# Performance work log

Hardware: AMD Instinct MI355X
Metric: run time of the kernel (lower is better)

The kernel has to match this reference:

```python
import jax, jax.numpy as jnp
import numpy as np

L = 2        # n_layer
D = 1024     # hidden_size
H = 8        # n_head
DK = D // H  # head_dim = 128
DV = D // H
T = 2048     # max_seq_length
B = 4
INTER = 2816 # fla GatedMLP: int(1024*4*2/3)=2730 rounded up to multiple of 256
EPS = 1e-6


def rmsnorm(x, w):
    return x * jax.lax.rsqrt(jnp.mean(x * x, axis=-1, keepdims=True) + EPS) * w


def l2norm(x):
    return x * jax.lax.rsqrt(jnp.sum(x * x, axis=-1, keepdims=True) + EPS)


def delta_attn(x, Wq, Wk, Wv, Wb, Wo, onorm_w):
    # x: [B, T, D]
    b, t, _ = x.shape
    q = jax.nn.silu((x @ Wq).reshape(b, t, H, DK))
    k = jax.nn.silu((x @ Wk).reshape(b, t, H, DK))
    q = l2norm(q)
    k = l2norm(k)
    v = jax.nn.silu((x @ Wv).reshape(b, t, H, DV))
    beta = jax.nn.sigmoid(x @ Wb) * 2.0  # [B,T,H], allow_neg_eigval=True
    # time-major for scan
    qt = q.transpose(1, 0, 2, 3)  # [T,B,H,DK]
    kt = k.transpose(1, 0, 2, 3)
    vt = v.transpose(1, 0, 2, 3)
    bt = beta.transpose(1, 0, 2)  # [T,B,H]

    def step(S, inps):
        qi, ki, vi, bi = inps
        # delta rule: S_t = S_{t-1} + beta_t * k_t (v_t - S_{t-1}^T k_t)^T
        pred = jnp.einsum('bhkv,bhk->bhv', S, ki)
        S = S + bi[..., None, None] * ki[..., :, None] * (vi - pred)[..., None, :]
        o = jnp.einsum('bhkv,bhk->bhv', S, qi)
        return S, o

    S0 = jnp.zeros((b, H, DK, DV), x.dtype)
    _, o = jax.lax.scan(step, S0, (qt, kt, vt, bt))  # o: [T,B,H,DV]
    o = rmsnorm(o, onorm_w)  # per-head RMSNorm (use_gate=False)
    o = o.transpose(1, 0, 2, 3).reshape(b, t, H * DV)
    return o @ Wo


def setup_inputs() -> dict:
    key = jax.random.key(0)
    ks = jax.random.split(key, 13)
    s = 0.02
    f32 = jnp.float32
    return {
        'input_embeds': jax.random.normal(ks[0], (T, B, D), f32),
        'Wq': jax.random.normal(ks[1], (L, D, D), f32) * s,
        'Wk': jax.random.normal(ks[2], (L, D, D), f32) * s,
        'Wv': jax.random.normal(ks[3], (L, D, D), f32) * s,
        'Wb': jax.random.normal(ks[4], (L, D, H), f32) * s,
        'Wo': jax.random.normal(ks[5], (L, D, D), f32) * s,
        'onorm_w': jnp.ones((L, DV), f32) + jax.random.normal(ks[6], (L, DV), f32) * 0.02,
        'norm1_w': jnp.ones((L, D), f32) + jax.random.normal(ks[7], (L, D), f32) * 0.02,
        'norm2_w': jnp.ones((L, D), f32) + jax.random.normal(ks[8], (L, D), f32) * 0.02,
        'Wg': jax.random.normal(ks[9], (L, D, 2 * INTER), f32) * s,
        'Wd': jax.random.normal(ks[10], (L, INTER, D), f32) * s,
        'final_norm_w': jnp.ones((D,), f32) + jax.random.normal(ks[11], (D,), f32) * 0.02,
    }


def reference(input_embeds, Wq, Wk, Wv, Wb, Wo, onorm_w, norm1_w, norm2_w, Wg, Wd, final_norm_w):
    # wrapper transposes (T,B,D) -> (B,T,D)
    x = input_embeds.transpose(1, 0, 2)
    for l in range(L):
        h = rmsnorm(x, norm1_w[l])
        x = x + delta_attn(h, Wq[l], Wk[l], Wv[l], Wb[l], Wo[l], onorm_w[l])
        h = rmsnorm(x, norm2_w[l])
        gy = h @ Wg[l]
        g, y = jnp.split(gy, 2, axis=-1)
        x = x + (jax.nn.silu(g) * y) @ Wd[l]
    x = rmsnorm(x, final_norm_w)
    return x.transpose(1, 0, 2)  # back to (T,B,D)
```

## Files before the change

kernel.cpp:

```cpp
#include <hip/hip_runtime.h>
#include <hip/hip_bf16.h>
#include <cstdint>


typedef _Float16 f16;
typedef __attribute__((ext_vector_type(8))) _Float16 h8;
typedef __attribute__((ext_vector_type(4))) _Float16 h4;
typedef __attribute__((ext_vector_type(4))) float f4;

#define DEV __device__ __forceinline__

static constexpr int Bb_ = 4;
static constexpr int Hh  = 8;
static constexpr int Dd  = 1024;
static constexpr int Tt  = 2048;
static constexpr int NC  = 32;

DEV float siluf(float x) { return x / (1.f + expf(-x)); }
DEV int swz16(int row, int c) { return (c & 8) | ((c & 7) ^ (row & 7)); }

#define AS1(p) ((const __attribute__((address_space(1))) void*)(uintptr_t)(p))
#define AS3(p) ((__attribute__((address_space(3))) void*)(uint32_t)(uintptr_t)(p))

DEV h8 rd_sw(const f16* T, int row, int chunk) {
  return *(const h8*)(T + (((row << 3) | (chunk ^ (row & 7))) * 8));
}

template<int EPI, int SC>
__global__ __launch_bounds__(512, 2) void gemm2(const f16* __restrict__ A, const f16* __restrict__ Bt,
                                                void* __restrict__ C, const float* __restrict__ rs,
                                                int M, int N, int K, int gx) {
  __shared__ __align__(16) f16 ldsA[2][16384];
  __shared__ __align__(16) f16 ldsB[2][8192];
  const int tid = threadIdx.x, lane = tid & 63, w = tid >> 6;
  const int l15 = lane & 15, l4 = lane >> 4;
  const int wr = w >> 2, wc = w & 3;
  const int nwg = gridDim.x;
  int flat = blockIdx.x;
  if ((nwg & 7) == 0) flat = (flat & 7) * (nwg >> 3) + (flat >> 3);
  const int bx = flat % gx, by = flat / gx;

  const f16* Ab = A + (size_t)by * 256 * K;
  const f16* Bb = Bt + (size_t)bx * 128 * K;
  const int NT = K >> 6;
  f4 acc[8][2] = {};

  const int r0 = tid >> 3;
  const size_t soff0 = (size_t)r0 * K + (size_t)(((tid & 7) ^ (r0 & 7)) * 8);
  const size_t soff1 = soff0 + (size_t)64 * K;
  const int dof = tid * 8;
  auto STG = [&](const f16* base, f16* dst) {
    __builtin_amdgcn_global_load_lds(AS1(base + soff0), AS3(dst + dof), 16, 0, 0);
    __builtin_amdgcn_global_load_lds(AS1(base + soff1), AS3(dst + 4096 + dof), 16, 0, 0);
  };

  STG(Bb, ldsB[0]);
  STG(Ab, ldsA[0]);
  STG(Ab + (size_t)128 * K, ldsA[0] + 8192);
  if (NT > 1) {
    STG(Bb + 64, ldsB[1]);
    asm volatile("s_waitcnt vmcnt(2)");
  } else {
    asm volatile("s_waitcnt vmcnt(0)");
  }
  __builtin_amdgcn_s_barrier();

  for (int t = 0; t < NT; ++t) {
    const int cur = t & 1, nxt = cur ^ 1;
    const f16* cA = ldsA[cur];
    const f16* cB = ldsB[cur];
    h8 b[2][2], aX[2][2], aY[2][2];
#pragma unroll
    for (int cf = 0; cf < 2; ++cf)
#pragma unroll
      for (int ks = 0; ks < 2; ++ks)
        b[cf][ks] = rd_sw(cB, wc * 32 + cf * 16 + l15, ks * 4 + l4);
#pragma unroll
    for (int fr = 0; fr < 2; ++fr)
#pragma unroll
      for (int ks = 0; ks < 2; ++ks)
        aX[fr][ks] = rd_sw(cA, wr * 128 + fr * 16 + l15, ks * 4 + l4);
    if (t + 1 < NT) { STG(Ab + (t + 1) * 64, ldsA[nxt]); STG(Ab + (size_t)128 * K + (t + 1) * 64, ldsA[nxt] + 8192); }
    __builtin_amdgcn_s_setprio(1);
#pragma unroll
    for (int fr = 0; fr < 2; ++fr)
#pragma unroll
      for (int cf = 0; cf < 2; ++cf)
#pragma unroll
        for (int ks = 0; ks < 2; ++ks)
          acc[fr][cf] = __builtin_amdgcn_mfma_f32_16x16x32_f16(aX[fr][ks], b[cf][ks], acc[fr][cf], 0, 0, 0);
#pragma unroll
    for (int fr = 0; fr < 2; ++fr)
#pragma unroll
      for (int ks = 0; ks < 2; ++ks)
        aY[fr][ks] = rd_sw(cA, wr * 128 + 32 + fr * 16 + l15, ks * 4 + l4);
#pragma unroll
    for (int fr = 0; fr < 2; ++fr)
#pragma unroll
      for (int cf = 0; cf < 2; ++cf)
#pragma unroll
        for (int ks = 0; ks < 2; ++ks)
          acc[2 + fr][cf] = __builtin_amdgcn_mfma_f32_16x16x32_f16(aY[fr][ks], b[cf][ks], acc[2 + fr][cf], 0, 0, 0);
    __builtin_amdgcn_s_setprio(0);
    __builtin_amdgcn_s_barrier();
#pragma unroll
    for (int fr = 0; fr < 2; ++fr)
#pragma unroll
      for (int ks = 0; ks < 2; ++ks)
        aX[fr][ks] = rd_sw(cA, wr * 128 + 64 + fr * 16 + l15, ks * 4 + l4);
    if (t + 2 < NT) STG(Bb + (t + 2) * 64, ldsB[cur]);
    __builtin_amdgcn_s_setprio(1);
#pragma unroll
    for (int fr = 0; fr < 2; ++fr)
#pragma unroll
      for (int cf = 0; cf < 2; ++cf)
#pragma unroll
        for (int ks = 0; ks < 2; ++ks)
          acc[4 + fr][cf] = __builtin_amdgcn_mfma_f32_16x16x32_f16(aX[fr][ks], b[cf][ks], acc[4 + fr][cf], 0, 0, 0);
#pragma unroll
    for (int fr = 0; fr < 2; ++fr)
#pragma unroll
      for (int ks = 0; ks < 2; ++ks)
        aY[fr][ks] = rd_sw(cA, wr * 128 + 96 + fr * 16 + l15, ks * 4 + l4);
#pragma unroll
    for (int fr = 0; fr < 2; ++fr)
#pragma unroll
      for (int cf = 0; cf < 2; ++cf)
#pragma unroll
        for (int ks = 0; ks < 2; ++ks)
          acc[6 + fr][cf] = __builtin_amdgcn_mfma_f32_16x16x32_f16(aY[fr][ks], b[cf][ks], acc[6 + fr][cf], 0, 0, 0);
    __builtin_amdgcn_s_setprio(0);
    if (t + 2 < NT)      asm volatile("s_waitcnt vmcnt(2)" ::: "memory");
    else if (t + 1 < NT) asm volatile("s_waitcnt vmcnt(0)" ::: "memory");
    __builtin_amdgcn_s_barrier();
  }

#pragma unroll
  for (int fr = 0; fr < 8; ++fr) {
#pragma unroll
    for (int cf = 0; cf < 2; ++cf) {
      const int row0 = by * 256 + wr * 128 + fr * 16 + l4 * 4;
      const int col = bx * 128 + wc * 32 + cf * 16 + l15;
#pragma unroll
      for (int q = 0; q < 4; ++q) {
        const size_t idx = (size_t)(row0 + q) * N + col;
        float v = acc[fr][cf][q];
        if (SC) v *= rs[row0 + q];
        if (EPI == 1) ((f16*)C)[idx] = (f16)((float)((f16*)C)[idx] + v);
        if (EPI == 2) ((f16*)C)[idx] = (f16)v;
      }
    }
  }
}

__global__ __launch_bounds__(512, 2) void gemmQKV(const f16* __restrict__ A, const f16* __restrict__ Bt,
                                                  const float* __restrict__ rs, f16* __restrict__ qb,
                                                  f16* __restrict__ kb, f16* __restrict__ vb,
                                                  int K, int gx) {
  __shared__ __align__(16) f16 ldsA[2][16384];
  __shared__ __align__(16) f16 ldsB[2][8192];
  __shared__ float ps[4][256];
  const int tid = threadIdx.x, lane = tid & 63, w = tid >> 6;
  const int l15 = lane & 15, l4 = lane >> 4;
  const int wr = w >> 2, wc = w & 3;
  const int nwg = gridDim.x;
  int flat = blockIdx.x;
  if ((nwg & 7) == 0) flat = (flat & 7) * (nwg >> 3) + (flat >> 3);
  const int bx = flat % gx, by = flat / gx;

  const f16* Ab = A + (size_t)by * 256 * K;
  const f16* Bb = Bt + (size_t)bx * 128 * K;
  const int NT = K >> 6;
  f4 acc[8][2] = {};

  const int r0 = tid >> 3;
  const size_t soff0 = (size_t)r0 * K + (size_t)(((tid & 7) ^ (r0 & 7)) * 8);
  const size_t soff1 = soff0 + (size_t)64 * K;
  const int dof = tid * 8;
  auto STG = [&](const f16* base, f16* dst) {
    __builtin_amdgcn_global_load_lds(AS1(base + soff0), AS3(dst + dof), 16, 0, 0);
    __builtin_amdgcn_global_load_lds(AS1(base + soff1), AS3(dst + 4096 + dof), 16, 0, 0);
  };

  STG(Bb, ldsB[0]);
  STG(Ab, ldsA[0]);
  STG(Ab + (size_t)128 * K, ldsA[0] + 8192);
  if (NT > 1) {
    STG(Bb + 64, ldsB[1]);
    asm volatile("s_waitcnt vmcnt(2)");
  } else {
    asm volatile("s_waitcnt vmcnt(0)");
  }
  __builtin_amdgcn_s_barrier();

  for (int t = 0; t < NT; ++t) {
    const int cur = t & 1, nxt = cur ^ 1;
    const f16* cA = ldsA[cur];
    const f16* cB = ldsB[cur];
    h8 b[2][2], aX[2][2], aY[2][2];
#pragma unroll
    for (int cf = 0; cf < 2; ++cf)
#pragma unroll
      for (int ks = 0; ks < 2; ++ks)
        b[cf][ks] = rd_sw(cB, wc * 32 + cf * 16 + l15, ks * 4 + l4);
#pragma unroll
    for (int fr = 0; fr < 2; ++fr)
#pragma unroll
      for (int ks = 0; ks < 2; ++ks)
        aX[fr][ks] = rd_sw(cA, wr * 128 + fr * 16 + l15, ks * 4 + l4);
    if (t + 1 < NT) { STG(Ab + (t + 1) * 64, ldsA[nxt]); STG(Ab + (size_t)128 * K + (t + 1) * 64, ldsA[nxt] + 8192); }
    __builtin_amdgcn_s_setprio(1);
#pragma unroll
    for (int fr = 0; fr < 2; ++fr)
#pragma unroll
      for (int cf = 0; cf < 2; ++cf)
#pragma unroll
        for (int ks = 0; ks < 2; ++ks)
          acc[fr][cf] = __builtin_amdgcn_mfma_f32_16x16x32_f16(aX[fr][ks], b[cf][ks], acc[fr][cf], 0, 0, 0);
#pragma unroll
    for (int fr = 0; fr < 2; ++fr)
#pragma unroll
      for (int ks = 0; ks < 2; ++ks)
        aY[fr][ks] = rd_sw(cA, wr * 128 + 32 + fr * 16 + l15, ks * 4 + l4);
#pragma unroll
    for (int fr = 0; fr < 2; ++fr)
#pragma unroll
      for (int cf = 0; cf < 2; ++cf)
#pragma unroll
        for (int ks = 0; ks < 2; ++ks)
          acc[2 + fr][cf] = __builtin_amdgcn_mfma_f32_16x16x32_f16(aY[fr][ks], b[cf][ks], acc[2 + fr][cf], 0, 0, 0);
    __builtin_amdgcn_s_setprio(0);
    __builtin_amdgcn_s_barrier();
#pragma unroll
    for (int fr = 0; fr < 2; ++fr)
#pragma unroll
      for (int ks = 0; ks < 2; ++ks)
        aX[fr][ks] = rd_sw(cA, wr * 128 + 64 + fr * 16 + l15, ks * 4 + l4);
    if (t + 2 < NT) STG(Bb + (t + 2) * 64, ldsB[cur]);
    __builtin_amdgcn_s_setprio(1);
#pragma unroll
    for (int fr = 0; fr < 2; ++fr)
#pragma unroll
      for (int cf = 0; cf < 2; ++cf)
#pragma unroll
        for (int ks = 0; ks < 2; ++ks)
          acc[4 + fr][cf] = __builtin_amdgcn_mfma_f32_16x16x32_f16(aX[fr][ks], b[cf][ks], acc[4 + fr][cf], 0, 0, 0);
#pragma unroll
    for (int fr = 0; fr < 2; ++fr)
#pragma unroll
      for (int ks = 0; ks < 2; ++ks)
        aY[fr][ks] = rd_sw(cA, wr * 128 + 96 + fr * 16 + l15, ks * 4 + l4);
#pragma unroll
    for (int fr = 0; fr < 2; ++fr)
#pragma unroll
      for (int cf = 0; cf < 2; ++cf)
#pragma unroll
        for (int ks = 0; ks < 2; ++ks)
          acc[6 + fr][cf] = __builtin_amdgcn_mfma_f32_16x16x32_f16(aY[fr][ks], b[cf][ks], acc[6 + fr][cf], 0, 0, 0);
    __builtin_amdgcn_s_setprio(0);
    if (t + 2 < NT)      asm volatile("s_waitcnt vmcnt(2)" ::: "memory");
    else if (t + 1 < NT) asm volatile("s_waitcnt vmcnt(0)" ::: "memory");
    __builtin_amdgcn_s_barrier();
  }

#pragma unroll
  for (int fr = 0; fr < 8; ++fr)
#pragma unroll
    for (int q = 0; q < 4; ++q) {
      const int grow = by * 256 + wr * 128 + fr * 16 + l4 * 4 + q;
      const float s = rs[grow];
#pragma unroll
      for (int cf = 0; cf < 2; ++cf)
        acc[fr][cf][q] = siluf(s * acc[fr][cf][q]);
    }
  if (bx < 16) {
    float sq[8][4];
#pragma unroll
    for (int fr = 0; fr < 8; ++fr)
#pragma unroll
      for (int q = 0; q < 4; ++q) {
        float v = acc[fr][0][q] * acc[fr][0][q] + acc[fr][1][q] * acc[fr][1][q];
#pragma unroll
        for (int m = 1; m < 16; m <<= 1) v += __shfl_xor(v, m);
        sq[fr][q] = v;
      }
    if (l15 == 0) {
#pragma unroll
      for (int fr = 0; fr < 8; ++fr)
#pragma unroll
        for (int q = 0; q < 4; ++q)
          ps[wc][wr * 128 + fr * 16 + l4 * 4 + q] = sq[fr][q];
    }
    __syncthreads();
#pragma unroll
    for (int fr = 0; fr < 8; ++fr)
#pragma unroll
      for (int q = 0; q < 4; ++q) {
        const int rl = wr * 128 + fr * 16 + l4 * 4 + q;
        const float sc = rsqrtf(ps[0][rl] + ps[1][rl] + ps[2][rl] + ps[3][rl] + 1e-6f);
#pragma unroll
        for (int cf = 0; cf < 2; ++cf) acc[fr][cf][q] *= sc;
      }
  }
  f16* dst = (bx < 8) ? qb : ((bx < 16) ? kb : vb);
  const int head = bx & 7;
#pragma unroll
  for (int fr = 0; fr < 8; ++fr)
#pragma unroll
    for (int cf = 0; cf < 2; ++cf)
#pragma unroll
      for (int q = 0; q < 4; ++q) {
        const int grow = by * 256 + wr * 128 + fr * 16 + l4 * 4 + q;
        const int i = (grow >> 2) & 63;
        const int dh = wc * 32 + cf * 16 + l15;
        dst[(size_t)grow * 1024 + head * 128 + swz16(i, dh >> 3) * 8 + (dh & 7)] = (f16)acc[fr][cf][q];
      }
}

__global__ __launch_bounds__(512, 2) void gemmGLU(const f16* __restrict__ A, const f16* __restrict__ WgT,
                                                  const float* __restrict__ rs, f16* __restrict__ my,
                                                  int K, int gx) {
  __shared__ __align__(16) f16 ldsA[2][16384];
  __shared__ __align__(16) f16 ldsG[2][8192];
  __shared__ __align__(16) f16 ldsY[2][8192];
  const int tid = threadIdx.x, lane = tid & 63, w = tid >> 6;
  const int l15 = lane & 15, l4 = lane >> 4;
  const int wr = w >> 2, wc = w & 3;
  const int nwg = gridDim.x;
  int flat = blockIdx.x;
  if ((nwg & 7) == 0) flat = (flat & 7) * (nwg >> 3) + (flat >> 3);
  const int bx = flat % gx, by = flat / gx;

  const f16* Ab = A + (size_t)by * 256 * K;
  const f16* Gb = WgT + (size_t)bx * 128 * K;
  const f16* Yb = WgT + (size_t)(2816 + bx * 128) * K;
  const int NT = K >> 6;
  f4 accG[8][2] = {}, accY[8][2] = {};

  const int r0 = tid >> 3;
  const size_t soff0 = (size_t)r0 * K + (size_t)(((tid & 7) ^ (r0 & 7)) * 8);
  const size_t soff1 = soff0 + (size_t)64 * K;
  const int dof = tid * 8;
  auto STG = [&](const f16* base, f16* dst) {
    __builtin_amdgcn_global_load_lds(AS1(base + soff0), AS3(dst + dof), 16, 0, 0);
    __builtin_amdgcn_global_load_lds(AS1(base + soff1), AS3(dst + 4096 + dof), 16, 0, 0);
  };

  STG(Gb, ldsG[0]);
  STG(Yb, ldsY[0]);
  STG(Ab, ldsA[0]);
  STG(Ab + (size_t)128 * K, ldsA[0] + 8192);
  if (NT > 1) {
    STG(Gb + 64, ldsG[1]);
    STG(Yb + 64, ldsY[1]);
    asm volatile("s_waitcnt vmcnt(4)");
  } else {
    asm volatile("s_waitcnt vmcnt(0)");
  }
  __builtin_amdgcn_s_barrier();

  for (int t = 0; t < NT; ++t) {
    const int cur = t & 1, nxt = cur ^ 1;
    const f16* cA = ldsA[cur];
    h8 bg[2][2], byv[2][2], aX[2][2], aY[2][2];
#pragma unroll
    for (int cf = 0; cf < 2; ++cf)
#pragma unroll
      for (int ks = 0; ks < 2; ++ks) {
        bg[cf][ks] = rd_sw(ldsG[cur], wc * 32 + cf * 16 + l15, ks * 4 + l4);
        byv[cf][ks] = rd_sw(ldsY[cur], wc * 32 + cf * 16 + l15, ks * 4 + l4);
      }
#pragma unroll
    for (int fr = 0; fr < 2; ++fr)
#pragma unroll
      for (int ks = 0; ks < 2; ++ks)
        aX[fr][ks] = rd_sw(cA, wr * 128 + fr * 16 + l15, ks * 4 + l4);
    if (t + 1 < NT) { STG(Ab + (t + 1) * 64, ldsA[nxt]); STG(Ab + (size_t)128 * K + (t + 1) * 64, ldsA[nxt] + 8192); }
    __builtin_amdgcn_s_setprio(1);
#pragma unroll
    for (int fr = 0; fr < 2; ++fr)
#pragma unroll
      for (int cf = 0; cf < 2; ++cf)
#pragma unroll
        for (int ks = 0; ks < 2; ++ks) {
          accG[fr][cf] = __builtin_amdgcn_mfma_f32_16x16x32_f16(aX[fr][ks], bg[cf][ks], accG[fr][cf], 0, 0, 0);
          accY[fr][cf] = __builtin_amdgcn_mfma_f32_16x16x32_f16(aX[fr][ks], byv[cf][ks], accY[fr][cf], 0, 0, 0);
        }
#pragma unroll
    for (int fr = 0; fr < 2; ++fr)
#pragma unroll
      for (int ks = 0; ks < 2; ++ks)
        aY[fr][ks] = rd_sw(cA, wr * 128 + 32 + fr * 16 + l15, ks * 4 + l4);
#pragma unroll
    for (int fr = 0; fr < 2; ++fr)
#pragma unroll
      for (int cf = 0; cf < 2; ++cf)
#pragma unroll
        for (int ks = 0; ks < 2; ++ks) {
          accG[2 + fr][cf] = __builtin_amdgcn_mfma_f32_16x16x32_f16(aY[fr][ks], bg[cf][ks], accG[2 + fr][cf], 0, 0, 0);
          accY[2 + fr][cf] = __builtin_amdgcn_mfma_f32_16x16x32_f16(aY[fr][ks], byv[cf][ks], accY[2 + fr][cf], 0, 0, 0);
        }
    __builtin_amdgcn_s_setprio(0);
    __builtin_amdgcn_s_barrier();
#pragma unroll
    for (int fr = 0; fr < 2; ++fr)
#pragma unroll
      for (int ks = 0; ks < 2; ++ks)
        aX[fr][ks] = rd_sw(cA, wr * 128 + 64 + fr * 16 + l15, ks * 4 + l4);
    if (t + 2 < NT) { STG(Gb + (t + 2) * 64, ldsG[cur]); STG(Yb + (t + 2) * 64, ldsY[cur]); }
    __builtin_amdgcn_s_setprio(1);
#pragma unroll
    for (int fr = 0; fr < 2; ++fr)
#pragma unroll
      for (int cf = 0; cf < 2; ++cf)
#pragma unroll
        for (int ks = 0; ks < 2; ++ks) {
          accG[4 + fr][cf] = __builtin_amdgcn_mfma_f32_16x16x32_f16(aX[fr][ks], bg[cf][ks], accG[4 + fr][cf], 0, 0, 0);
          accY[4 + fr][cf] = __builtin_amdgcn_mfma_f32_16x16x32_f16(aX[fr][ks], byv[cf][ks], accY[4 + fr][cf], 0, 0, 0);
        }
#pragma unroll
    for (int fr = 0; fr < 2; ++fr)
#pragma unroll
      for (int ks = 0; ks < 2; ++ks)
        aY[fr][ks] = rd_sw(cA, wr * 128 + 96 + fr * 16 + l15, ks * 4 + l4);
#pragma unroll
    for (int fr = 0; fr < 2; ++fr)
#pragma unroll
      for (int cf = 0; cf < 2; ++cf)
#pragma unroll
        for (int ks = 0; ks < 2; ++ks) {
          accG[6 + fr][cf] = __builtin_amdgcn_mfma_f32_16x16x32_f16(aY[fr][ks], bg[cf][ks], accG[6 + fr][cf], 0, 0, 0);
          accY[6 + fr][cf] = __builtin_amdgcn_mfma_f32_16x16x32_f16(aY[fr][ks], byv[cf][ks], accY[6 + fr][cf], 0, 0, 0);
        }
    __builtin_amdgcn_s_setprio(0);
    if (t + 2 < NT)      asm volatile("s_waitcnt vmcnt(4)" ::: "memory");
    else if (t + 1 < NT) asm volatile("s_waitcnt vmcnt(0)" ::: "memory");
    __builtin_amdgcn_s_barrier();
  }

#pragma unroll
  for (int fr = 0; fr < 8; ++fr) {
#pragma unroll
    for (int cf = 0; cf < 2; ++cf) {
      const int row0 = by * 256 + wr * 128 + fr * 16 + l4 * 4;
      const int col = bx * 128 + wc * 32 + cf * 16 + l15;
#pragma unroll
      for (int q = 0; q < 4; ++q) {
        const float s = rs[row0 + q];
        my[(size_t)(row0 + q) * 2816 + col] = (f16)(siluf(s * accG[fr][cf][q]) * (s * accY[fr][cf][q]));
      }
    }
  }
}

__global__ __launch_bounds__(256) void cvt_k(const float* __restrict__ in, f16* __restrict__ out) {
  const size_t i = ((size_t)blockIdx.x * 256 + threadIdx.x) * 8;
  const float4 a = *(const float4*)(in + i);
  const float4 b = *(const float4*)(in + i + 4);
  h8 o = {(f16)a.x, (f16)a.y, (f16)a.z, (f16)a.w, (f16)b.x, (f16)b.y, (f16)b.z, (f16)b.w};
  *(h8*)(out + i) = o;
}

__global__ __launch_bounds__(256) void rowscale_k(const f16* __restrict__ x, float* __restrict__ rs) {
  const int tid = threadIdx.x, lane = tid & 63, wv = tid >> 6;
  const int r = blockIdx.x * 4 + wv;
  const f16* row = x + (size_t)r * 1024 + lane * 16;
  const h8 v0 = *(const h8*)(row);
  const h8 v1 = *(const h8*)(row + 8);
  float ss = 0.f;
#pragma unroll
  for (int e = 0; e < 8; ++e) {
    const float a = (float)v0[e], b = (float)v1[e];
    ss += a * a + b * b;
  }
#pragma unroll
  for (int m = 1; m < 64; m <<= 1) ss += __shfl_xor(ss, m);
  if (lane == 0) rs[r] = rsqrtf(ss * (1.f / 1024.f) + 1e-6f);
}

__global__ __launch_bounds__(256) void rmsnorm_f(const f16* __restrict__ x, const float* __restrict__ w,
                                                 float* __restrict__ out) {
  const int r = blockIdx.x, tid = threadIdx.x;
  const h4 xv = *(const h4*)(x + (size_t)r * 1024 + tid * 4);
  const float v0 = (float)xv[0], v1 = (float)xv[1], v2 = (float)xv[2], v3 = (float)xv[3];
  float ss = v0 * v0 + v1 * v1 + v2 * v2 + v3 * v3;
#pragma unroll
  for (int m = 1; m < 64; m <<= 1) ss += __shfl_xor(ss, m);
  __shared__ float red[4];
  if ((tid & 63) == 0) red[tid >> 6] = ss;
  __syncthreads();
  const float scale = rsqrtf((red[0] + red[1] + red[2] + red[3]) * (1.f / 1024.f) + 1e-6f);
  const float4 w4 = *(const float4*)(w + tid * 4);
  *(float4*)(out + (size_t)r * 1024 + tid * 4) =
      make_float4(v0 * scale * w4.x, v1 * scale * w4.y, v2 * scale * w4.z, v3 * scale * w4.w);
}

__global__ __launch_bounds__(256) void onorm_k(const f16* __restrict__ o, const float* __restrict__ w,
                                               f16* __restrict__ ob) {
  const int r = blockIdx.x, tid = threadIdx.x;
  const int head = tid >> 5, l32 = tid & 31;
  const size_t base = (size_t)r * 1024 + head * 128 + l32 * 4;
  const h4 xv = *(const h4*)(o + base);
  const float v0 = (float)xv[0], v1 = (float)xv[1], v2 = (float)xv[2], v3 = (float)xv[3];
  float ss = v0 * v0 + v1 * v1 + v2 * v2 + v3 * v3;
#pragma unroll
  for (int m = 1; m <= 16; m <<= 1) ss += __shfl_xor(ss, m);
  const float sc = rsqrtf(ss * (1.f / 128.f) + 1e-6f);
  const float4 w4 = *(const float4*)(w + l32 * 4);
  h4 out = {(f16)(v0 * sc * w4.x), (f16)(v1 * sc * w4.y), (f16)(v2 * sc * w4.z), (f16)(v3 * sc * w4.w)};
  *(h4*)(ob + base) = out;
}

__global__ __launch_bounds__(256) void beta_k(const f16* __restrict__ x, const float* __restrict__ Wb2,
                                              const float* __restrict__ rs, float* __restrict__ beta) {
  const int tid = threadIdx.x, lane = tid & 63, wv = tid >> 6;
  const int r = blockIdx.x * 4 + wv;
  const f16* row = x + (size_t)r * 1024 + lane * 16;
  const h8 v0 = *(const h8*)(row);
  const h8 v1 = *(const h8*)(row + 8);
  const float* wb = Wb2 + (size_t)(lane * 16) * 8;
  float acc[8] = {};
#pragma unroll
  for (int e = 0; e < 8; ++e) {
    const float x0 = (float)v0[e], x1 = (float)v1[e];
    const float4 w0a = *(const float4*)(wb + e * 8);
    const float4 w0b = *(const float4*)(wb + e * 8 + 4);
    const float4 w1a = *(const float4*)(wb + (e + 8) * 8);
    const float4 w1b = *(const float4*)(wb + (e + 8) * 8 + 4);
    acc[0] += x0 * w0a.x + x1 * w1a.x;  acc[1] += x0 * w0a.y + x1 * w1a.y;
    acc[2] += x0 * w0a.z + x1 * w1a.z;  acc[3] += x0 * w0a.w + x1 * w1a.w;
    acc[4] += x0 * w0b.x + x1 * w1b.x;  acc[5] += x0 * w0b.y + x1 * w1b.y;
    acc[6] += x0 * w0b.z + x1 * w1b.z;  acc[7] += x0 * w0b.w + x1 * w1b.w;
  }
#pragma unroll
  for (int j = 0; j < 8; ++j)
#pragma unroll
    for (int m = 1; m < 64; m <<= 1) acc[j] += __shfl_xor(acc[j], m);
  if (lane == 0) {
    const float s = rs[r];
#pragma unroll
    for (int j = 0; j < 8; ++j) beta[(size_t)r * 8 + j] = 2.f / (1.f + expf(-acc[j] * s));
  }
}

template<int FOLD>
__global__ __launch_bounds__(256) void transpose_k(const float* __restrict__ W, const float* __restrict__ rw,
                                                   f16* __restrict__ Wt, int K, int N) {
  __shared__ float tile[32][33];
  const int n0 = blockIdx.x * 32, k0 = blockIdx.y * 32;
  const int tx = threadIdx.x & 31, ty = threadIdx.x >> 5;
#pragma unroll
  for (int i = 0; i < 32; i += 8) {
    float v = W[(size_t)(k0 + ty + i) * N + n0 + tx];
    if (FOLD) v *= rw[k0 + ty + i];
    tile[ty + i][tx] = v;
  }
  __syncthreads();
#pragma unroll
  for (int i = 0; i < 32; i += 8) Wt[(size_t)(n0 + ty + i) * K + k0 + tx] = (f16)tile[tx][ty + i];
}

__global__ __launch_bounds__(256) void bweight_k(const float* __restrict__ Wb, const float* __restrict__ n1w,
                                                 float* __restrict__ Wb2) {
  const int idx = blockIdx.x * 256 + threadIdx.x;
  Wb2[idx] = Wb[idx] * n1w[idx >> 3];
}

__global__ void fill_k(float* p, int n, float v) {
  const int i = blockIdx.x * 256 + threadIdx.x;
  if (i < n) p[i] = v;
}

DEV f4 mm16(const f16* A, int as, const f16* B, f4 c, int l15, int l4) {
  h4 a = *(const h4*)(A + l15 * as + l4 * 4);
  h4 b = *(const h4*)(B + l15 * 20 + l4 * 4);
  return __builtin_amdgcn_mfma_f32_16x16x16f16(a, b, c, 0, 0, 0);
}
DEV void wr_T(f16* slot, f4 acc, int l15, int l4, float sgn) {
  h4 v = {(f16)(sgn * acc[0]), (f16)(sgn * acc[1]), (f16)(sgn * acc[2]), (f16)(sgn * acc[3])};
  *(h4*)(slot + l15 * 20 + l4 * 4) = v;
}
DEV void wr_Tb(f16* Tb, int bi, int bj, f4 acc, const float* betas, int l15, int l4, float sgn) {
  const float bc = betas[bj * 16 + l15];
#pragma unroll
  for (int q = 0; q < 4; ++q)
    Tb[(bi * 16 + l4 * 4 + q) * 72 + bj * 16 + l15] = (f16)(sgn * acc[q] * bc);
}

__global__ __launch_bounds__(256) void phaseA(const f16* __restrict__ kb, const f16* __restrict__ qb,
                                              const f16* __restrict__ vb, const float* __restrict__ beta,
                                              f16* __restrict__ wbuf, f16* __restrict__ utbuf,
                                              f16* __restrict__ pbuf, f16* __restrict__ ktbuf) {
  const int blk = blockIdx.x;
  const int c = blk >> 5, bh = blk & 31;
  const int b = bh >> 3, h = bh & 7;
  const int tid = threadIdx.x, lane = tid & 63, wv = tid >> 6;
  const int l15 = lane & 15, l4 = lane >> 4;

  __shared__ __align__(16) f16 Ks[64 * 128];
  __shared__ __align__(16) f16 QVs[64 * 128];
  __shared__ __align__(16) f16 Abuf[64 * 68];
  __shared__ __align__(16) f16 Dr[4][16 * 20];
  __shared__ __align__(16) f16 Dt[4][16 * 20];
  __shared__ __align__(16) f16 Tp[3][16 * 20];
  __shared__ __align__(16) f16 Xp[3][16 * 20];
  __shared__ __align__(16) f16 Tb[64 * 72];
  __shared__ float betas[64];

  const size_t rowstr = (size_t)Bb_ * Dd;
  const size_t gbase = ((size_t)(c * 64) * Bb_ + b) * Dd + h * 128;

#pragma unroll
  for (int i = 0; i < 4; ++i) {
    const int ch = tid + i * 256;
    const int rr = ch >> 4, kc = ch & 15;
    *(h8*)(Ks + ch * 8) = *(const h8*)(kb + gbase + (size_t)rr * rowstr + kc * 8);
    *(h8*)(QVs + ch * 8) = *(const h8*)(qb + gbase + (size_t)rr * rowstr + kc * 8);
  }
  for (int i = tid; i < 64 * 72; i += 256) Tb[i] = (f16)0.f;
  if (tid < 64) betas[tid] = beta[((size_t)(c * 64 + tid) * Bb_ + b) * Hh + h];
  __syncthreads();

  f4 accS[4] = {}, accP[4] = {};
  const int arow = wv * 16 + l15;
#pragma unroll
  for (int kc = 0; kc < 4; ++kc) {
    const int c4 = kc * 4 + l4;
    const h8 aK = *(const h8*)(Ks + arow * 128 + swz16(arow, c4) * 8);
    const h8 aQ = *(const h8*)(QVs + arow * 128 + swz16(arow, c4) * 8);
#pragma unroll
    for (int f = 0; f < 4; ++f) {
      const int brow = f * 16 + l15;
      const h8 bK = *(const h8*)(Ks + brow * 128 + swz16(brow, c4) * 8);
      accS[f] = __builtin_amdgcn_mfma_f32_16x16x32_f16(aK, bK, accS[f], 0, 0, 0);
      accP[f] = __builtin_amdgcn_mfma_f32_16x16x32_f16(aQ, bK, accP[f], 0, 0, 0);
    }
  }
  const size_t pbase = (((size_t)bh * NC + c) * 64) * 64;
#pragma unroll
  for (int f = 0; f < 4; ++f) {
#pragma unroll
    for (int q = 0; q < 4; ++q) {
      const int i = wv * 16 + l4 * 4 + q;
      const int j = f * 16 + l15;
      Abuf[i * 68 + j] = (f16)((j < i) ? betas[i] * accS[f][q] : 0.f);
      pbuf[pbase + (size_t)i * 64 + j] = (f16)((j <= i) ? accP[f][q] : 0.f);
    }
  }
  __syncthreads();

#pragma unroll
  for (int i = 0; i < 4; ++i) {
    const int ch = tid + i * 256;
    const int rr = ch >> 4, kc = ch & 15;
    *(h8*)(QVs + ch * 8) = *(const h8*)(vb + gbase + (size_t)rr * rowstr + kc * 8);
  }

  {
    const int bi = wv;
    const int cc = l15;
    const f16* Ad = Abuf + (bi * 16) * 68 + bi * 16;
    float t[16];
    t[0] = (cc == 0) ? 1.f : 0.f;
#pragma unroll
    for (int i = 1; i < 16; ++i) {
      float s = (cc == i) ? 1.f : 0.f;
#pragma unroll
      for (int j = 0; j < i; ++j) s -= (float)Ad[i * 68 + j] * t[j];
      t[i] = s;
    }
    if (lane < 16) {
#pragma unroll
      for (int j4 = 0; j4 < 4; ++j4) {
        h4 v = {(f16)t[j4 * 4], (f16)t[j4 * 4 + 1], (f16)t[j4 * 4 + 2], (f16)t[j4 * 4 + 3]};
        *(h4*)(&Dt[bi][cc * 20 + j4 * 4]) = v;
      }
      const float bc = betas[bi * 16 + cc];
#pragma unroll
      for (int j = 0; j < 16; ++j) {
        Dr[bi][j * 20 + cc] = (f16)t[j];
        Tb[(bi * 16 + j) * 72 + bi * 16 + cc] = (f16)(t[j] * bc);
      }
    }
  }
  __syncthreads();

  const f16* AB10 = Abuf + 16 * 68 + 0;
  const f16* AB20 = Abuf + 32 * 68 + 0;
  const f16* AB21 = Abuf + 32 * 68 + 16;
  const f16* AB30 = Abuf + 48 * 68 + 0;
  const f16* AB31 = Abuf + 48 * 68 + 16;
  const f16* AB32 = Abuf + 48 * 68 + 32;
  f4 z = {};
  f4 x20, x30;

  if (wv == 0) wr_T(Xp[0], mm16(AB10, 68, Dt[0], z, l15, l4), l15, l4, 1.f);
  if (wv == 1) wr_T(Xp[1], mm16(AB21, 68, Dt[1], z, l15, l4), l15, l4, 1.f);
  if (wv == 2) wr_T(Xp[2], mm16(AB32, 68, Dt[2], z, l15, l4), l15, l4, 1.f);
  if (wv == 3) x20 = mm16(AB20, 68, Dt[0], z, l15, l4);
  __syncthreads();
  if (wv == 0) { f4 r = mm16(Dr[1], 20, Xp[0], z, l15, l4); wr_T(Tp[0], r, l15, l4, -1.f); wr_Tb(Tb, 1, 0, r, betas, l15, l4, -1.f); }
  if (wv == 1) { f4 r = mm16(Dr[2], 20, Xp[1], z, l15, l4); wr_T(Tp[1], r, l15, l4, -1.f); wr_Tb(Tb, 2, 1, r, betas, l15, l4, -1.f); }
  if (wv == 2) { f4 r = mm16(Dr[3], 20, Xp[2], z, l15, l4); wr_Tb(Tb, 3, 2, r, betas, l15, l4, -1.f); }
  if (wv == 3) x30 = mm16(AB30, 68, Dt[0], z, l15, l4);
  __syncthreads();
  if (wv == 3) wr_T(Xp[0], mm16(AB21, 68, Tp[0], x20, l15, l4), l15, l4, 1.f);
  if (wv == 1) { f4 r = mm16(AB31, 68, Dt[1], z, l15, l4); r = mm16(AB32, 68, Tp[1], r, l15, l4); wr_T(Xp[1], r, l15, l4, 1.f); }
  __syncthreads();
  if (wv == 3) { f4 r = mm16(Dr[2], 20, Xp[0], z, l15, l4); wr_T(Tp[2], r, l15, l4, -1.f); wr_Tb(Tb, 2, 0, r, betas, l15, l4, -1.f); }
  if (wv == 1) { f4 r = mm16(Dr[3], 20, Xp[1], z, l15, l4); wr_Tb(Tb, 3, 1, r, betas, l15, l4, -1.f); }
  __syncthreads();
  if (wv == 3) { f4 r = mm16(AB31, 68, Tp[0], x30, l15, l4); r = mm16(AB32, 68, Tp[2], r, l15, l4); wr_T(Xp[2], r, l15, l4, 1.f); }
  __syncthreads();
  if (wv == 3) { f4 r = mm16(Dr[3], 20, Xp[2], z, l15, l4); wr_Tb(Tb, 3, 0, r, betas, l15, l4, -1.f); }
  __syncthreads();

  const size_t wub = ((size_t)bh * NC + c) * 8192;
  const int koff = l4 * 8;
  f4 wacc[8] = {}, uacc[8] = {};
#pragma unroll
  for (int kc = 0; kc < 2; ++kc) {
    const h8 aT = *(const h8*)(Tb + (wv * 16 + l15) * 72 + kc * 32 + koff);
#pragma unroll
    for (int f = 0; f < 8; ++f) {
      const int d = f * 16 + l15, cD = d >> 3, d7 = d & 7;
      h8 bK, bV;
#pragma unroll
      for (int j = 0; j < 8; ++j) {
        const int t2 = kc * 32 + koff + j;
        const int pos = t2 * 128 + swz16(t2, cD) * 8 + d7;
        bK[j] = Ks[pos];
        bV[j] = QVs[pos];
      }
      wacc[f] = __builtin_amdgcn_mfma_f32_16x16x32_f16(aT, bK, wacc[f], 0, 0, 0);
      uacc[f] = __builtin_amdgcn_mfma_f32_16x16x32_f16(aT, bV, uacc[f], 0, 0, 0);
    }
  }
#pragma unroll
  for (int f = 0; f < 8; ++f) {
// ... 206 lines not shown
```

Measured before the change: 943.6 us.

## Replace double-buffered LDS staging with single buffer in GEMM kernels

Replaces the double-buffered LDS staging in the three GEMM kernels with one buffer. Each k-step now loads all fragments into registers first, then issues the next tile's global-to-LDS copies and overlaps them with the second half of the MFMA work. This halves LDS use per block, which may allow more resident blocks. In exchange, the loads now only overlap half a tile of MFMA work and need extra barriers and waits per iteration, so memory latency is less well hidden.

```diff
diff --git a/kernel.cpp b/kernel.cpp
--- a/kernel.cpp
+++ b/kernel.cpp
@@ -30,8 +30,8 @@
 __global__ __launch_bounds__(512, 2) void gemm2(const f16* __restrict__ A, const f16* __restrict__ Bt,
                                                 void* __restrict__ C, const float* __restrict__ rs,
                                                 int M, int N, int K, int gx) {
-  __shared__ __align__(16) f16 ldsA[2][16384];
-  __shared__ __align__(16) f16 ldsB[2][8192];
+  __shared__ __align__(16) f16 ldsA[16384];
+  __shared__ __align__(16) f16 ldsB[8192];
   const int tid = threadIdx.x, lane = tid & 63, w = tid >> 6;
   const int l15 = lane & 15, l4 = lane >> 4;
   const int wr = w >> 2, wc = w & 3;
@@ -54,84 +54,64 @@
     __builtin_amdgcn_global_load_lds(AS1(base + soff1), AS3(dst + 4096 + dof), 16, 0, 0);
   };
 
-  STG(Bb, ldsB[0]);
-  STG(Ab, ldsA[0]);
-  STG(Ab + (size_t)128 * K, ldsA[0] + 8192);
-  if (NT > 1) {
-    STG(Bb + 64, ldsB[1]);
-    asm volatile("s_waitcnt vmcnt(2)");
-  } else {
-    asm volatile("s_waitcnt vmcnt(0)");
-  }
+  STG(Bb, ldsB);
+  STG(Ab, ldsA);
+  STG(Ab + (size_t)128 * K, ldsA + 8192);
+  asm volatile("s_waitcnt vmcnt(0)" ::: "memory");
   __builtin_amdgcn_s_barrier();
 
   for (int t = 0; t < NT; ++t) {
-    const int cur = t & 1, nxt = cur ^ 1;
-    const f16* cA = ldsA[cur];
-    const f16* cB = ldsB[cur];
     h8 b[2][2], aX[2][2], aY[2][2];
 #pragma unroll
     for (int cf = 0; cf < 2; ++cf)
 #pragma unroll
       for (int ks = 0; ks < 2; ++ks)
-        b[cf][ks] = rd_sw(cB, wc * 32 + cf * 16 + l15, ks * 4 + l4);
-#pragma unroll
-    for (int fr = 0; fr < 2; ++fr)
-#pragma unroll
-      for (int ks = 0; ks < 2; ++ks)
-        aX[fr][ks] = rd_sw(cA, wr * 128 + fr * 16 + l15, ks * 4 + l4);
-    if (t + 1 < NT) { STG(Ab + (t + 1) * 64, ldsA[nxt]); STG(Ab + (size_t)128 * K + (t + 1) * 64, ldsA[nxt] + 8192); }
+        b[cf][ks] = rd_sw(ldsB, wc * 32 + cf * 16 + l15, ks * 4 + l4);
+#pragma unroll
+    for (int fr = 0; fr < 2; ++fr)
+#pragma unroll
+      for (int ks = 0; ks < 2; ++ks) {
+        aX[fr][ks] = rd_sw(ldsA, wr * 128 + fr * 16 + l15, ks * 4 + l4);
+        aY[fr][ks] = rd_sw(ldsA, wr * 128 + 32 + fr * 16 + l15, ks * 4 + l4);
+      }
     __builtin_amdgcn_s_setprio(1);
 #pragma unroll
     for (int fr = 0; fr < 2; ++fr)
 #pragma unroll
       for (int cf = 0; cf < 2; ++cf)
 #pragma unroll
-        for (int ks = 0; ks < 2; ++ks)
+        for (int ks = 0; ks < 2; ++ks) {
           acc[fr][cf] = __builtin_amdgcn_mfma_f32_16x16x32_f16(aX[fr][ks], b[cf][ks], acc[fr][cf], 0, 0, 0);
-#pragma unroll
-    for (int fr = 0; fr < 2; ++fr)
-#pragma unroll
-      for (int ks = 0; ks < 2; ++ks)
-        aY[fr][ks] = rd_sw(cA, wr * 128 + 32 + fr * 16 + l15, ks * 4 + l4);
+          acc[2 + fr][cf] = __builtin_amdgcn_mfma_f32_16x16x32_f16(aY[fr][ks], b[cf][ks], acc[2 + fr][cf], 0, 0, 0);
+        }
+    __builtin_amdgcn_s_setprio(0);
+    __builtin_amdgcn_s_barrier();
+#pragma unroll
+    for (int fr = 0; fr < 2; ++fr)
+#pragma unroll
+      for (int ks = 0; ks < 2; ++ks) {
+        aX[fr][ks] = rd_sw(ldsA, wr * 128 + 64 + fr * 16 + l15, ks * 4 + l4);
+        aY[fr][ks] = rd_sw(ldsA, wr * 128 + 96 + fr * 16 + l15, ks * 4 + l4);
+      }
+    asm volatile("s_waitcnt lgkmcnt(0)" ::: "memory");
+    __builtin_amdgcn_s_barrier();
+    if (t + 1 < NT) {
+      STG(Ab + (t + 1) * 64, ldsA);
+      STG(Ab + (size_t)128 * K + (t + 1) * 64, ldsA + 8192);
+      STG(Bb + (t + 1) * 64, ldsB);
+    }
+    __builtin_amdgcn_s_setprio(1);
 #pragma unroll
     for (int fr = 0; fr < 2; ++fr)
 #pragma unroll
       for (int cf = 0; cf < 2; ++cf)
 #pragma unroll
-        for (int ks = 0; ks < 2; ++ks)
-          acc[2 + fr][cf] = __builtin_amdgcn_mfma_f32_16x16x32_f16(aY[fr][ks], b[cf][ks], acc[2 + fr][cf], 0, 0, 0);
+        for (int ks = 0; ks < 2; ++ks) {
+          acc[4 + fr][cf] = __builtin_amdgcn_mfma_f32_16x16x32_f16(aX[fr][ks], b[cf][ks], acc[4 + fr][cf], 0, 0, 0);
+          acc[6 + fr][cf] = __builtin_amdgcn_mfma_f32_16x16x32_f16(aY[fr][ks], b[cf][ks], acc[6 + fr][cf], 0, 0, 0);
+        }
     __builtin_amdgcn_s_setprio(0);
-    __builtin_amdgcn_s_barrier();
-#pragma unroll
-    for (int fr = 0; fr < 2; ++fr)
-#pragma unroll
-      for (int ks = 0; ks < 2; ++ks)
-        aX[fr][ks] = rd_sw(cA, wr * 128 + 64 + fr * 16 + l15, ks * 4 + l4);
-    if (t + 2 < NT) STG(Bb + (t + 2) * 64, ldsB[cur]);
-    __builtin_amdgcn_s_setprio(1);
-#pragma unroll
-    for (int fr = 0; fr < 2; ++fr)
-#pragma unroll
-      for (int cf = 0; cf < 2; ++cf)
-#pragma unroll
-        for (int ks = 0; ks < 2; ++ks)
-          acc[4 + fr][cf] = __builtin_amdgcn_mfma_f32_16x16x32_f16(aX[fr][ks], b[cf][ks], acc[4 + fr][cf], 0, 0, 0);
-#pragma unroll
-    for (int fr = 0; fr < 2; ++fr)
-#pragma unroll
-      for (int ks = 0; ks < 2; ++ks)
-        aY[fr][ks] = rd_sw(cA, wr * 128 + 96 + fr * 16 + l15, ks * 4 + l4);
-#pragma unroll
-    for (int fr = 0; fr < 2; ++fr)
-#pragma unroll
-      for (int cf = 0; cf < 2; ++cf)
-#pragma unroll
-        for (int ks = 0; ks < 2; ++ks)
-          acc[6 + fr][cf] = __builtin_amdgcn_mfma_f32_16x16x32_f16(aY[fr][ks], b[cf][ks], acc[6 + fr][cf], 0, 0, 0);
-    __builtin_amdgcn_s_setprio(0);
-    if (t + 2 < NT)      asm volatile("s_waitcnt vmcnt(2)" ::: "memory");
-    else if (t + 1 < NT) asm volatile("s_waitcnt vmcnt(0)" ::: "memory");
+    if (t + 1 < NT) asm volatile("s_waitcnt vmcnt(0)" ::: "memory");
     __builtin_amdgcn_s_barrier();
   }
 
@@ -157,8 +137,8 @@
                                                   const float* __restrict__ rs, f16* __restrict__ qb,
                                                   f16* __restrict__ kb, f16* __restrict__ vb,
                                                   int K, int gx) {
-  __shared__ __align__(16) f16 ldsA[2][16384];
-  __shared__ __align__(16) f16 ldsB[2][8192];
+  __shared__ __align__(16) f16 ldsA[16384];
+  __shared__ __align__(16) f16 ldsB[8192];
   __shared__ float ps[4][256];
   const int tid = threadIdx.x, lane = tid & 63, w = tid >> 6;
   const int l15 = lane & 15, l4 = lane >> 4;
@@ -182,84 +162,64 @@
     __builtin_amdgcn_global_load_lds(AS1(base + soff1), AS3(dst + 4096 + dof), 16, 0, 0);
   };
 
-  STG(Bb, ldsB[0]);
-  STG(Ab, ldsA[0]);
-  STG(Ab + (size_t)128 * K, ldsA[0] + 8192);
-  if (NT > 1) {
-    STG(Bb + 64, ldsB[1]);
-    asm volatile("s_waitcnt vmcnt(2)");
-  } else {
-    asm volatile("s_waitcnt vmcnt(0)");
-  }
+  STG(Bb, ldsB);
+  STG(Ab, ldsA);
+  STG(Ab + (size_t)128 * K, ldsA + 8192);
+  asm volatile("s_waitcnt vmcnt(0)" ::: "memory");
   __builtin_amdgcn_s_barrier();
 
   for (int t = 0; t < NT; ++t) {
-    const int cur = t & 1, nxt = cur ^ 1;
-    const f16* cA = ldsA[cur];
-    const f16* cB = ldsB[cur];
     h8 b[2][2], aX[2][2], aY[2][2];
 #pragma unroll
     for (int cf = 0; cf < 2; ++cf)
 #pragma unroll
       for (int ks = 0; ks < 2; ++ks)
-        b[cf][ks] = rd_sw(cB, wc * 32 + cf * 16 + l15, ks * 4 + l4);
-#pragma unroll
-    for (int fr = 0; fr < 2; ++fr)
-#pragma unroll
-      for (int ks = 0; ks < 2; ++ks)
-        aX[fr][ks] = rd_sw(cA, wr * 128 + fr * 16 + l15, ks * 4 + l4);
-    if (t + 1 < NT) { STG(Ab + (t + 1) * 64, ldsA[nxt]); STG(Ab + (size_t)128 * K + (t + 1) * 64, ldsA[nxt] + 8192); }
+        b[cf][ks] = rd_sw(ldsB, wc * 32 + cf * 16 + l15, ks * 4 + l4);
+#pragma unroll
+    for (int fr = 0; fr < 2; ++fr)
+#pragma unroll
+      for (int ks = 0; ks < 2; ++ks) {
+        aX[fr][ks] = rd_sw(ldsA, wr * 128 + fr * 16 + l15, ks * 4 + l4);
+        aY[fr][ks] = rd_sw(ldsA, wr * 128 + 32 + fr * 16 + l15, ks * 4 + l4);
+      }
     __builtin_amdgcn_s_setprio(1);
 #pragma unroll
     for (int fr = 0; fr < 2; ++fr)
 #pragma unroll
       for (int cf = 0; cf < 2; ++cf)
 #pragma unroll
-        for (int ks = 0; ks < 2; ++ks)
+        for (int ks = 0; ks < 2; ++ks) {
           acc[fr][cf] = __builtin_amdgcn_mfma_f32_16x16x32_f16(aX[fr][ks], b[cf][ks], acc[fr][cf], 0, 0, 0);
-#pragma unroll
-    for (int fr = 0; fr < 2; ++fr)
-#pragma unroll
-      for (int ks = 0; ks < 2; ++ks)
-        aY[fr][ks] = rd_sw(cA, wr * 128 + 32 + fr * 16 + l15, ks * 4 + l4);
+          acc[2 + fr][cf] = __builtin_amdgcn_mfma_f32_16x16x32_f16(aY[fr][ks], b[cf][ks], acc[2 + fr][cf], 0, 0, 0);
+        }
+    __builtin_amdgcn_s_setprio(0);
+    __builtin_amdgcn_s_barrier();
+#pragma unroll
+    for (int fr = 0; fr < 2; ++fr)
+#pragma unroll
+      for (int ks = 0; ks < 2; ++ks) {
+        aX[fr][ks] = rd_sw(ldsA, wr * 128 + 64 + fr * 16 + l15, ks * 4 + l4);
+        aY[fr][ks] = rd_sw(ldsA, wr * 128 + 96 + fr * 16 + l15, ks * 4 + l4);
+      }
+    asm volatile("s_waitcnt lgkmcnt(0)" ::: "memory");
+    __builtin_amdgcn_s_barrier();
+    if (t + 1 < NT) {
+      STG(Ab + (t + 1) * 64, ldsA);
+      STG(Ab + (size_t)128 * K + (t + 1) * 64, ldsA + 8192);
+      STG(Bb + (t + 1) * 64, ldsB);
+    }
+    __builtin_amdgcn_s_setprio(1);
 #pragma unroll
     for (int fr = 0; fr < 2; ++fr)
 #pragma unroll
       for (int cf = 0; cf < 2; ++cf)
 #pragma unroll
-        for (int ks = 0; ks < 2; ++ks)
-          acc[2 + fr][cf] = __builtin_amdgcn_mfma_f32_16x16x32_f16(aY[fr][ks], b[cf][ks], acc[2 + fr][cf], 0, 0, 0);
+        for (int ks = 0; ks < 2; ++ks) {
+          acc[4 + fr][cf] = __builtin_amdgcn_mfma_f32_16x16x32_f16(aX[fr][ks], b[cf][ks], acc[4 + fr][cf], 0, 0, 0);
+          acc[6 + fr][cf] = __builtin_amdgcn_mfma_f32_16x16x32_f16(aY[fr][ks], b[cf][ks], acc[6 + fr][cf], 0, 0, 0);
+        }
     __builtin_amdgcn_s_setprio(0);
-    __builtin_amdgcn_s_barrier();
-#pragma unroll
-    for (int fr = 0; fr < 2; ++fr)
-#pragma unroll
-      for (int ks = 0; ks < 2; ++ks)
-        aX[fr][ks] = rd_sw(cA, wr * 128 + 64 + fr * 16 + l15, ks * 4 + l4);
-    if (t + 2 < NT) STG(Bb + (t + 2) * 64, ldsB[cur]);
-    __builtin_amdgcn_s_setprio(1);
-#pragma unroll
-    for (int fr = 0; fr < 2; ++fr)
-#pragma unroll
-      for (int cf = 0; cf < 2; ++cf)
-#pragma unroll
-        for (int ks = 0; ks < 2; ++ks)
-          acc[4 + fr][cf] = __builtin_amdgcn_mfma_f32_16x16x32_f16(aX[fr][ks], b[cf][ks], acc[4 + fr][cf], 0, 0, 0);
-#pragma unroll
-    for (int fr = 0; fr < 2; ++fr)
-#pragma unroll
-      for (int ks = 0; ks < 2; ++ks)
-        aY[fr][ks] = rd_sw(cA, wr * 128 + 96 + fr * 16 + l15, ks * 4 + l4);
-#pragma unroll
-    for (int fr = 0; fr < 2; ++fr)
-#pragma unroll
-      for (int cf = 0; cf < 2; ++cf)
-#pragma unroll
-        for (int ks = 0; ks < 2; ++ks)
-          acc[6 + fr][cf] = __builtin_amdgcn_mfma_f32_16x16x32_f16(aY[fr][ks], b[cf][ks], acc[6 + fr][cf], 0, 0, 0);
-    __builtin_amdgcn_s_setprio(0);
-    if (t + 2 < NT)      asm volatile("s_waitcnt vmcnt(2)" ::: "memory");
-    else if (t + 1 < NT) asm volatile("s_waitcnt vmcnt(0)" ::: "memory");
+    if (t + 1 < NT) asm volatile("s_waitcnt vmcnt(0)" ::: "memory");
     __builtin_amdgcn_s_barrier();
   }
 
@@ -320,9 +280,9 @@
 __global__ __launch_bounds__(512, 2) void gemmGLU(const f16* __restrict__ A, const f16* __restrict__ WgT,
                                                   const float* __restrict__ rs, f16* __restrict__ my,
                                                   int K, int gx) {
-  __shared__ __align__(16) f16 ldsA[2][16384];
-  __shared__ __align__(16) f16 ldsG[2][8192];
-  __shared__ __align__(16) f16 ldsY[2][8192];
+  __shared__ __align__(16) f16 ldsA[16384];
+  __shared__ __align__(16) f16 ldsG[8192];
+  __shared__ __align__(16) f16 ldsY[8192];
   const int tid = threadIdx.x, lane = tid & 63, w = tid >> 6;
   const int l15 = lane & 15, l4 = lane >> 4;
   const int wr = w >> 2, wc = w & 3;
@@ -346,36 +306,29 @@
     __builtin_amdgcn_global_load_lds(AS1(base + soff1), AS3(dst + 4096 + dof), 16, 0, 0);
   };
 
-  STG(Gb, ldsG[0]);
-  STG(Yb, ldsY[0]);
-  STG(Ab, ldsA[0]);
-  STG(Ab + (size_t)128 * K, ldsA[0] + 8192);
-  if (NT > 1) {
-    STG(Gb + 64, ldsG[1]);
-    STG(Yb + 64, ldsY[1]);
-    asm volatile("s_waitcnt vmcnt(4)");
-  } else {
-    asm volatile("s_waitcnt vmcnt(0)");
-  }
+  STG(Gb, ldsG);
+  STG(Yb, ldsY);
+  STG(Ab, ldsA);
+  STG(Ab + (size_t)128 * K, ldsA + 8192);
+  asm volatile("s_waitcnt vmcnt(0)" ::: "memory");
   __builtin_amdgcn_s_barrier();
 
   for (int t = 0; t < NT; ++t) {
-    const int cur = t & 1, nxt = cur ^ 1;
-    const f16* cA = ldsA[cur];
     h8 bg[2][2], byv[2][2], aX[2][2], aY[2][2];
 #pragma unroll
     for (int cf = 0; cf < 2; ++cf)
 #pragma unroll
       for (int ks = 0; ks < 2; ++ks) {
-        bg[cf][ks] = rd_sw(ldsG[cur], wc * 32 + cf * 16 + l15, ks * 4 + l4);
-        byv[cf][ks] = rd_sw(ldsY[cur], wc * 32 + cf * 16 + l15, ks * 4 + l4);
-      }
-#pragma unroll
-    for (int fr = 0; fr < 2; ++fr)
-#pragma unroll
-      for (int ks = 0; ks < 2; ++ks)
-        aX[fr][ks] = rd_sw(cA, wr * 128 + fr * 16 + l15, ks * 4 + l4);
-    if (t + 1 < NT) { STG(Ab + (t + 1) * 64, ldsA[nxt]); STG(Ab + (size_t)128 * K + (t + 1) * 64, ldsA[nxt] + 8192); }
+        bg[cf][ks] = rd_sw(ldsG, wc * 32 + cf * 16 + l15, ks * 4 + l4);
+        byv[cf][ks] = rd_sw(ldsY, wc * 32 + cf * 16 + l15, ks * 4 + l4);
+      }
+#pragma unroll
+    for (int fr = 0; fr < 2; ++fr)
+#pragma unroll
+      for (int ks = 0; ks < 2; ++ks) {
+        aX[fr][ks] = rd_sw(ldsA, wr * 128 + fr * 16 + l15, ks * 4 + l4);
+        aY[fr][ks] = rd_sw(ldsA, wr * 128 + 32 + fr * 16 + l15, ks * 4 + l4);
+      }
     __builtin_amdgcn_s_setprio(1);
 #pragma unroll
     for (int fr = 0; fr < 2; ++fr)
@@ -385,18 +338,6 @@
         for (int ks = 0; ks < 2; ++ks) {
           accG[fr][cf] = __builtin_amdgcn_mfma_f32_16x16x32_f16(aX[fr][ks], bg[cf][ks], accG[fr][cf], 0, 0, 0);
           accY[fr][cf] = __builtin_amdgcn_mfma_f32_16x16x32_f16(aX[fr][ks], byv[cf][ks], accY[fr][cf], 0, 0, 0);
-        }
-#pragma unroll
-    for (int fr = 0; fr < 2; ++fr)
-#pragma unroll
-      for (int ks = 0; ks < 2; ++ks)
-        aY[fr][ks] = rd_sw(cA, wr * 128 + 32 + fr * 16 + l15, ks * 4 + l4);
-#pragma unroll
-    for (int fr = 0; fr < 2; ++fr)
-#pragma unroll
-      for (int cf = 0; cf < 2; ++cf)
-#pragma unroll
-        for (int ks = 0; ks < 2; ++ks) {
           accG[2 + fr][cf] = __builtin_amdgcn_mfma_f32_16x16x32_f16(aY[fr][ks], bg[cf][ks], accG[2 + fr][cf], 0, 0, 0);
           accY[2 + fr][cf] = __builtin_amdgcn_mfma_f32_16x16x32_f16(aY[fr][ks], byv[cf][ks], accY[2 + fr][cf], 0, 0, 0);
         }
@@ -405,9 +346,18 @@
 #pragma unroll
     for (int fr = 0; fr < 2; ++fr)
 #pragma unroll
-      for (int ks = 0; ks < 2; ++ks)
-        aX[fr][ks] = rd_sw(cA, wr * 128 + 64 + fr * 16 + l15, ks * 4 + l4);
-    if (t + 2 < NT) { STG(Gb + (t + 2) * 64, ldsG[cur]); STG(Yb + (t + 2) * 64, ldsY[cur]); }
+      for (int ks = 0; ks < 2; ++ks) {
+        aX[fr][ks] = rd_sw(ldsA, wr * 128 + 64 + fr * 16 + l15, ks * 4 + l4);
+        aY[fr][ks] = rd_sw(ldsA, wr * 128 + 96 + fr * 16 + l15, ks * 4 + l4);
+      }
+    asm volatile("s_waitcnt lgkmcnt(0)" ::: "memory");
+    __builtin_amdgcn_s_barrier();
+    if (t + 1 < NT) {
+      STG(Ab + (t + 1) * 64, ldsA);
+      STG(Ab + (size_t)128 * K + (t + 1) * 64, ldsA + 8192);
+      STG(Gb + (t + 1) * 64, ldsG);
+      STG(Yb + (t + 1) * 64, ldsY);
+    }
     __builtin_amdgcn_s_setprio(1);
 #pragma unroll
     for (int fr = 0; fr < 2; ++fr)
@@ -417,24 +367,11 @@
         for (int ks = 0; ks < 2; ++ks) {
           accG[4 + fr][cf] = __builtin_amdgcn_mfma_f32_16x16x32_f16(aX[fr][ks], bg[cf][ks], accG[4 + fr][cf], 0, 0, 0);
           accY[4 + fr][cf] = __builtin_amdgcn_mfma_f32_16x16x32_f16(aX[fr][ks], byv[cf][ks], accY[4 + fr][cf], 0, 0, 0);
-        }
-#pragma unroll
-    for (int fr = 0; fr < 2; ++fr)
-#pragma unroll
-      for (int ks = 0; ks < 2; ++ks)
-        aY[fr][ks] = rd_sw(cA, wr * 128 + 96 + fr * 16 + l15, ks * 4 + l4);
-#pragma unroll
-    for (int fr = 0; fr < 2; ++fr)
-#pragma unroll
-      for (int cf = 0; cf < 2; ++cf)
-#pragma unroll
-        for (int ks = 0; ks < 2; ++ks) {
           accG[6 + fr][cf] = __builtin_amdgcn_mfma_f32_16x16x32_f16(aY[fr][ks], bg[cf][ks], accG[6 + fr][cf], 0, 0, 0);
           accY[6 + fr][cf] = __builtin_amdgcn_mfma_f32_16x16x32_f16(aY[fr][ks], byv[cf][ks], accY[6 + fr][cf], 0, 0, 0);
         }
     __builtin_amdgcn_s_setprio(0);
-    if (t + 2 < NT)      asm volatile("s_waitcnt vmcnt(4)" ::: "memory");
-    else if (t + 1 < NT) asm volatile("s_waitcnt vmcnt(0)" ::: "memory");
+    if (t + 1 < NT) asm volatile("s_waitcnt vmcnt(0)" ::: "memory");
     __builtin_amdgcn_s_barrier();
   }
 
```

New measurement: 970.6 us. 2.9% more time.
